# Kernel tuning notes

Measured on AMD Instinct MI355X. Metric: run time of the kernel, lower is better.

Reference implementation:

```python
import jax, jax.numpy as jnp
import numpy as np

B, S, D = 4, 4096, 256


def setup_inputs() -> dict:
    key = jax.random.key(0)
    k1, k2, k3 = jax.random.split(key, 3)
    x = jax.random.normal(k1, (B, S, D), dtype=jnp.float32)
    w_int = jax.random.randint(k2, (D, D), 0, 127, dtype=jnp.int32)  # quantized weight (out, in)
    scale = jax.random.uniform(k3, (D,), dtype=jnp.float32)          # per-output-channel scale
    return {"x": x, "w_int": w_int, "scale": scale}


def reference(x, w_int, scale):
    # self-attention: q = k = v = x, single head over feature dim D
    inv_sqrt_d = 1.0 / jnp.sqrt(jnp.asarray(D, dtype=x.dtype))
    scores = jnp.einsum('bqd,bkd->bqk', x, x) * inv_sqrt_d   # [B,S,S]
    probs = jax.nn.softmax(scores, axis=-1)
    attn = jnp.einsum('bqk,bkd->bqd', probs, x)              # [B,S,D]
    # quantized linear: dequantize then matmul (y = attn @ W^T)
    W = w_int.astype(x.dtype) * scale[:, None]               # [D_out, D_in]
    return jnp.einsum('bsd,od->bso', attn, W)
```

## Files before the change

### kernel.cpp

```cpp
#include <hip/hip_runtime.h>

typedef __bf16 bf16x8 __attribute__((ext_vector_type(8)));
typedef float f32x16 __attribute__((ext_vector_type(16)));
typedef unsigned short u16x8 __attribute__((ext_vector_type(8)));

constexpr int B = 4, S = 4096, D = 256;
constexpr float CSC = 0.09016844005556021f;

static __device__ __forceinline__ unsigned short f2bf(float f) {
  unsigned int u = __builtin_bit_cast(unsigned int, f);
  u = (u + 0x7fffu + ((u >> 16) & 1u)) >> 16;
  return (unsigned short)u;
}

static __device__ __forceinline__ float bf2f(unsigned short u) {
  unsigned int v = ((unsigned int)u) << 16;
  return __builtin_bit_cast(float, v);
}

static __device__ __forceinline__ unsigned int pk2bf(float lo, float hi) {
  unsigned int r;
  asm("v_cvt_pk_bf16_f32 %0, %1, %2" : "=v"(r) : "v"(lo), "v"(hi));
  return r;
}

static __device__ __forceinline__ void gld16(const void* g, void* l) {
  __builtin_amdgcn_global_load_lds(
      (const __attribute__((address_space(1))) unsigned int*)g,
      (__attribute__((address_space(3))) unsigned int*)l, 16, 0, 0);
}

#define FENCE_ALL()                                               \
  do {                                                            \
    asm volatile("s_waitcnt vmcnt(0) lgkmcnt(0)" ::: "memory");   \
    __builtin_amdgcn_s_barrier();                                 \
    asm volatile("" ::: "memory");                                \
  } while (0)

__global__ __launch_bounds__(256) void k_prep(const float* __restrict__ x,
                                              unsigned short* __restrict__ xbf,
                                              unsigned short* __restrict__ xK,
                                              unsigned short* __restrict__ xV) {
  __shared__ unsigned short T[64][72];
  __shared__ unsigned short R[64][72];
  int bid = blockIdx.x;
  int b = bid >> 8, rem = bid & 255;
  int s0 = (rem >> 2) * 64, d0 = (rem & 3) * 64;
  int j = threadIdx.x & 63, i0 = threadIdx.x >> 6;
#pragma unroll
  for (int k = 0; k < 16; ++k) {
    int i = k * 4 + i0;
    int idx = (b * S + s0 + i) * D + d0 + j;
    unsigned short v = f2bf(x[idx]);
    xbf[idx] = v;
    T[j][i] = v;
    R[i][j] = v;
  }
  __syncthreads();
  int t = s0 >> 6;
#pragma unroll
  for (int p = 0; p < 2; ++p) {
    int cc = p * 256 + threadIdx.x;
    int sl8 = cc >> 6, row = cc & 63;
    u16x8 v = *(const u16x8*)&R[row][sl8 * 8];
    int dg = d0 + sl8 * 8;
    int s = dg >> 4, hi = (dg >> 3) & 1;
    size_t off = ((((size_t)(b * 64 + t) * 16 + s) * 2 + hi) * 64 + row) * 8;
    *(u16x8*)(xK + off) = v;
  }
#pragma unroll
  for (int p = 0; p < 2; ++p) {
    int cc = p * 256 + threadIdx.x;
    int c = cc >> 7, hi = (cc >> 6) & 1, dl = cc & 63;
    u16x8 v = *(const u16x8*)&T[dl][c * 16 + hi * 8];
    size_t off = ((((size_t)(b * 64 + t) * 4 + c) * 2 + hi) * 256 + (d0 + dl)) * 8;
    *(u16x8*)(xV + off) = v;
  }
}

__global__ __launch_bounds__(256) void k_deqw(const int* __restrict__ w,
                                              unsigned short* __restrict__ wK) {
  int o = blockIdx.x, d = threadIdx.x;
  unsigned short v = f2bf((float)w[o * 256 + d]);
  wK[(((d >> 4) * 2 + ((d >> 3) & 1)) * 256 + o) * 8 + (d & 7)] = v;
}

__global__ __launch_bounds__(512, 2) void k_attn(const unsigned short* __restrict__ xbf,
                                                 const unsigned short* __restrict__ xK,
                                                 const unsigned short* __restrict__ xV,
                                                 unsigned short* __restrict__ PO0,
                                                 unsigned short* __restrict__ PO1,
                                                 float* __restrict__ ML) {
  __shared__ __align__(16) char smem[132096];

  int tid = threadIdx.x;
  int w = tid >> 6, lane = tid & 63;
  int q5 = lane & 31, hi = lane >> 5;
  int pair = w >> 1, dh = w & 1;

  int bid = blockIdx.x;
  int swz = (bid & 7) * 32 + (bid >> 3);
  int h = swz & 1;
  int qg = swz >> 1;
  int q0 = qg * 128;
  int bat = q0 >> 12;
  int qloc = q0 & (S - 1);

  const unsigned short* Xb = xbf + (size_t)bat * (S * D);
  int qw = qloc + pair * 32;

  bf16x8 qf[16];
#pragma unroll
  for (int s = 0; s < 16; ++s)
    qf[s] = *(const bf16x8*)(Xb + (qw + q5) * D + s * 16 + hi * 8);

  f32x16 acc[8];
#pragma unroll
  for (int dt = 0; dt < 8; ++dt)
#pragma unroll
    for (int j = 0; j < 16; ++j) acc[dt][j] = 0.f;
  float l_lane = 0.f;

  const char* xKb = (const char*)xK + (size_t)(bat * 64 + h * 32) * 32768;
  const char* xVb = (const char*)xV + (size_t)(bat * 64 + h * 32) * 32768;

  auto STAGE = [&](int itile, int bb) {
    char* Kd = smem + bb * 32768;
    char* Vd = smem + 65536 + bb * 32768;
    const char* srcK = xKb + (size_t)itile * 32768;
    const char* srcV = xVb + (size_t)itile * 32768;
#pragma unroll
    for (int i = 0; i < 4; ++i) {
      int off = (w * 2 + (i >> 1)) * 2048 + (i & 1) * 1024;
      gld16(srcK + off + lane * 16, Kd + off);
    }
#pragma unroll
    for (int i = 0; i < 4; ++i) {
      int off = (w >> 1) * 8192 + ((w & 1) * 4 + i) * 1024;
      gld16(srcV + off + lane * 16, Vd + off);
    }
  };

  STAGE(0, 0);
  FENCE_ALL();

  for (int it = 0; it < 32; ++it) {
    int bb = it & 1;
    if (it + 1 < 32) STAGE(it + 1, bb ^ 1);

    const char* Kt = smem + bb * 32768 + hi * 1024 + dh * 512 + q5 * 16;
    f32x16 st;
#pragma unroll
    for (int j = 0; j < 16; ++j) st[j] = 0.f;
    __builtin_amdgcn_s_setprio(1);
#pragma unroll
    for (int s = 0; s < 16; ++s) {
      bf16x8 kf = *(const bf16x8*)(Kt + s * 2048);
      st = __builtin_amdgcn_mfma_f32_32x32x16_bf16(kf, qf[s], st, 0, 0, 0);
    }
    __builtin_amdgcn_s_setprio(0);

    unsigned int pk[8];
    float ps = 0.f;
#pragma unroll
    for (int a = 0; a < 8; ++a) {
      float lo = exp2f(st[2 * a] * CSC);
      float hh = exp2f(st[2 * a + 1] * CSC);
      ps += lo + hh;
      pk[a] = pk2bf(lo, hh);
    }
    l_lane += ps;

    unsigned int a0 = pk[0], b0 = pk[2];
    unsigned int a1 = pk[1], b1 = pk[3];
    unsigned int a2 = pk[4], b2 = pk[6];
    unsigned int a3 = pk[5], b3 = pk[7];
    asm volatile("v_permlane32_swap_b32 %0, %1" : "+v"(a0), "+v"(b0));
    asm volatile("v_permlane32_swap_b32 %0, %1" : "+v"(a1), "+v"(b1));
    asm volatile("v_permlane32_swap_b32 %0, %1" : "+v"(a2), "+v"(b2));
    asm volatile("v_permlane32_swap_b32 %0, %1" : "+v"(a3), "+v"(b3));
    union PA { unsigned int u[4]; bf16x8 v; };
    PA pa0, pa1;
    pa0.u[0] = a0; pa0.u[1] = a1; pa0.u[2] = b0; pa0.u[3] = b1;
    pa1.u[0] = a2; pa1.u[1] = a3; pa1.u[2] = b2; pa1.u[3] = b3;

    __builtin_amdgcn_s_setprio(1);
#pragma unroll
    for (int s2i = 0; s2i < 2; ++s2i) {
      const char* Vt = smem + 65536 + bb * 32768 + (dh * 2 + s2i) * 8192 +
                       hi * 4096 + q5 * 16;
      bf16x8 pa = (s2i == 0) ? pa0.v : pa1.v;
#pragma unroll
      for (int dt = 0; dt < 8; ++dt) {
        bf16x8 vf = *(const bf16x8*)(Vt + dt * 512);
        acc[dt] = __builtin_amdgcn_mfma_f32_32x32x16_bf16(vf, pa, acc[dt], 0, 0, 0);
      }
    }
    __builtin_amdgcn_s_setprio(0);

    FENCE_ALL();
  }

  float lw = l_lane + __shfl_xor(l_lane, 32, 64);
  float* LX = (float*)(smem + 131072);
  if (lane < 32) LX[w * 32 + q5] = lw;
  __syncthreads();
  float l_tot = lw + LX[(w ^ 1) * 32 + q5];
  if (dh == 0 && lane < 32) {
    int row = q0 + pair * 32 + q5;
    ML[((size_t)h * 16384 + row) * 2 + 0] = 0.f;
    ML[((size_t)h * 16384 + row) * 2 + 1] = l_tot;
  }
  __syncthreads();

  unsigned short* Pb2 = (h == 0) ? PO0 : PO1;
#pragma unroll
  for (int rh = 0; rh < 2; ++rh) {
    float* slot = (float*)(smem + w * 16384);
#pragma unroll
    for (int dt4 = 0; dt4 < 4; ++dt4) {
#pragma unroll
      for (int r = 0; r < 16; ++r) {
        int dloc = dt4 * 32 + (r & 3) + 8 * (r >> 2) + 4 * hi;
        slot[dloc * 32 + q5] = acc[rh * 4 + dt4][r];
      }
    }
    __syncthreads();
    if (dh == rh) {
      const float* pslot = (const float*)(smem + (w ^ 1) * 16384);
#pragma unroll
      for (int dt4 = 0; dt4 < 4; ++dt4) {
#pragma unroll
        for (int r = 0; r < 16; ++r) {
          int dloc = dt4 * 32 + (r & 3) + 8 * (r >> 2) + 4 * hi;
          acc[rh * 4 + dt4][r] += pslot[dloc * 32 + q5];
        }
      }
      char* E = smem + w * 16384;
#pragma unroll
      for (int dt4 = 0; dt4 < 4; ++dt4) {
#pragma unroll
        for (int a = 0; a < 4; ++a) {
          int dl = dt4 * 32 + 8 * a + 4 * hi;
          *(unsigned int*)(E + q5 * 272 + dl * 2) =
              pk2bf(acc[rh * 4 + dt4][4 * a + 0], acc[rh * 4 + dt4][4 * a + 1]);
          *(unsigned int*)(E + q5 * 272 + dl * 2 + 4) =
              pk2bf(acc[rh * 4 + dt4][4 * a + 2], acc[rh * 4 + dt4][4 * a + 3]);
        }
      }
      asm volatile("s_waitcnt lgkmcnt(0)" ::: "memory");
#pragma unroll
      for (int i = 0; i < 8; ++i) {
        int qr = i * 4 + (lane >> 4);
        int ch = lane & 15;
        u16x8 v = *(const u16x8*)(E + qr * 272 + ch * 16);
        *(u16x8*)(Pb2 + (size_t)(q0 + pair * 32 + qr) * 256 + rh * 128 + ch * 8) = v;
      }
    }
    __syncthreads();
  }
}

__global__ __launch_bounds__(512, 2) void k_gemm(const unsigned short* __restrict__ PO0,
                                                 const unsigned short* __restrict__ PO1,
                                                 const float* __restrict__ ML,
                                                 const unsigned short* __restrict__ wK,
                                                 const float* __restrict__ scale,
                                                 float* __restrict__ out) {
  __shared__ __align__(16) char Wl[131072];
  int tid = threadIdx.x;
  int w = tid >> 6, lane = tid & 63;
  int q5 = lane & 31, hi = lane >> 5;
  int msub = w & 1, oq = w >> 1;
  int m0 = blockIdx.x * 64;

#pragma unroll
  for (int i = 0; i < 16; ++i) {
    int off = (i * 512 + tid) * 16;
    gld16((const char*)wK + off, Wl + off);
  }

  int row = m0 + msub * 32 + q5;
  float il = 1.f / (ML[(size_t)row * 2 + 1] + ML[((size_t)16384 + row) * 2 + 1]);

  bf16x8 af[16];
#pragma unroll
  for (int s = 0; s < 16; ++s) {
    u16x8 a0 = *(const u16x8*)(PO0 + (size_t)row * 256 + s * 16 + hi * 8);
    u16x8 a1 = *(const u16x8*)(PO1 + (size_t)row * 256 + s * 16 + hi * 8);
    union { unsigned int u[4]; bf16x8 v; } cv;
#pragma unroll
    for (int e = 0; e < 4; ++e) {
      float lo = (bf2f(a0[2 * e]) + bf2f(a1[2 * e])) * il;
      float hh = (bf2f(a0[2 * e + 1]) + bf2f(a1[2 * e + 1])) * il;
      cv.u[e] = pk2bf(lo, hh);
    }
    af[s] = cv.v;
  }

  asm volatile("s_waitcnt vmcnt(0)" ::: "memory");
  __builtin_amdgcn_s_barrier();

  f32x16 acc[2];
#pragma unroll
  for (int t = 0; t < 2; ++t)
#pragma unroll
    for (int j = 0; j < 16; ++j) acc[t][j] = 0.f;

#pragma unroll
  for (int t = 0; t < 2; ++t) {
    int obase = (oq * 2 + t) * 32;
    const char* Wt = Wl + hi * 4096 + (obase + q5) * 16;
#pragma unroll
    for (int s = 0; s < 16; ++s) {
      bf16x8 wf = *(const bf16x8*)(Wt + s * 8192);
      acc[t] = __builtin_amdgcn_mfma_f32_32x32x16_bf16(af[s], wf, acc[t], 0, 0, 0);
    }
  }

#pragma unroll
  for (int t = 0; t < 2; ++t) {
    int o = (oq * 2 + t) * 32 + q5;
    float sc = scale[o];
#pragma unroll
    for (int r = 0; r < 16; ++r) {
      int mr = m0 + msub * 32 + (r & 3) + 8 * (r >> 2) + 4 * hi;
      out[(size_t)mr * 256 + o] = acc[t][r] * sc;
    }
  }
}

extern "C" void kernel_launch(void* const* d_in, const int* in_sizes, int n_in,
                              void* d_out, int out_size, void* d_ws, size_t ws_size,
                              hipStream_t stream) {
  (void)in_sizes; (void)n_in; (void)out_size; (void)ws_size;
  const float* x = (const float*)d_in[0];
  const int* w_int = (const int*)d_in[1];
  const float* scale = (const float*)d_in[2];
  float* out = (float*)d_out;

  char* ws = (char*)d_ws;
  unsigned short* xbf = (unsigned short*)(ws);
  unsigned short* xK  = (unsigned short*)(ws + 8388608);
  unsigned short* xV  = (unsigned short*)(ws + 16777216);
  unsigned short* wK  = (unsigned short*)(ws + 25165824);
  float*          ML  = (float*)(ws + 25296896);
  unsigned short* PO0 = (unsigned short*)(ws + 25821184);
  unsigned short* PO1 = (unsigned short*)(ws + 34209792);

  k_prep<<<dim3(1024), dim3(256), 0, stream>>>(x, xbf, xK, xV);
  k_deqw<<<dim3(256), dim3(256), 0, stream>>>(w_int, wK);
  k_attn<<<dim3(256), dim3(512), 0, stream>>>(xbf, xK, xV, PO0, PO1, ML);
  k_gemm<<<dim3(256), dim3(512), 0, stream>>>(PO0, PO1, ML, wK, scale, out);
}
```

Before: 104.3 us.

## Software-pipeline QK and PV across tiles and drop separate bf16 x copy

Restructures the attention loop so K and V tiles are staged separately with partial vmcnt waits. The QK^T of tile t now overlaps with the PV of tile t-1, with softmax probabilities carried in registers between iterations. This is meant to hide load latency and keep the MFMA pipe busy instead of fully draining memory every iteration. It also removes the row-major bf16 copy of x and reads Q fragments from the K-layout buffer, saving one 8 MB write and its workspace. It adds register pressure from the carried probabilities and makes the fence and vmcnt accounting more delicate.

```diff
diff --git a/kernel.cpp b/kernel.cpp
--- a/kernel.cpp
+++ b/kernel.cpp
@@ -30,7 +30,25 @@
       (__attribute__((address_space(3))) unsigned int*)l, 16, 0, 0);
 }
 
-#define FENCE_ALL()                                               \
+#define FENCE_V4()                                                \
+  do {                                                            \
+    asm volatile("s_waitcnt vmcnt(4) lgkmcnt(0)" ::: "memory");   \
+    __builtin_amdgcn_s_barrier();                                 \
+    asm volatile("" ::: "memory");                                \
+  } while (0)
+#define FENCE_V8()                                                \
+  do {                                                            \
+    asm volatile("s_waitcnt vmcnt(8) lgkmcnt(0)" ::: "memory");   \
+    __builtin_amdgcn_s_barrier();                                 \
+    asm volatile("" ::: "memory");                                \
+  } while (0)
+#define FENCE_LG()                                                \
+  do {                                                            \
+    asm volatile("s_waitcnt lgkmcnt(0)" ::: "memory");            \
+    __builtin_amdgcn_s_barrier();                                 \
+    asm volatile("" ::: "memory");                                \
+  } while (0)
+#define FENCE_ALL0()                                              \
   do {                                                            \
     asm volatile("s_waitcnt vmcnt(0) lgkmcnt(0)" ::: "memory");   \
     __builtin_amdgcn_s_barrier();                                 \
@@ -38,7 +56,6 @@
   } while (0)
 
 __global__ __launch_bounds__(256) void k_prep(const float* __restrict__ x,
-                                              unsigned short* __restrict__ xbf,
                                               unsigned short* __restrict__ xK,
                                               unsigned short* __restrict__ xV) {
   __shared__ unsigned short T[64][72];
@@ -52,7 +69,6 @@
     int i = k * 4 + i0;
     int idx = (b * S + s0 + i) * D + d0 + j;
     unsigned short v = f2bf(x[idx]);
-    xbf[idx] = v;
     T[j][i] = v;
     R[i][j] = v;
   }
@@ -85,8 +101,7 @@
   wK[(((d >> 4) * 2 + ((d >> 3) & 1)) * 256 + o) * 8 + (d & 7)] = v;
 }
 
-__global__ __launch_bounds__(512, 2) void k_attn(const unsigned short* __restrict__ xbf,
-                                                 const unsigned short* __restrict__ xK,
+__global__ __launch_bounds__(512, 2) void k_attn(const unsigned short* __restrict__ xK,
                                                  const unsigned short* __restrict__ xV,
                                                  unsigned short* __restrict__ PO0,
                                                  unsigned short* __restrict__ PO1,
@@ -106,13 +121,12 @@
   int bat = q0 >> 12;
   int qloc = q0 & (S - 1);
 
-  const unsigned short* Xb = xbf + (size_t)bat * (S * D);
-  int qw = qloc + pair * 32;
-
+  int qrow = qloc + pair * 32 + q5;
+  const unsigned short* Qb =
+      xK + (size_t)(bat * 64 + (qrow >> 6)) * 16384 + hi * 512 + (qrow & 63) * 8;
   bf16x8 qf[16];
 #pragma unroll
-  for (int s = 0; s < 16; ++s)
-    qf[s] = *(const bf16x8*)(Xb + (qw + q5) * D + s * 16 + hi * 8);
+  for (int s = 0; s < 16; ++s) qf[s] = *(const bf16x8*)(Qb + s * 1024);
 
   f32x16 acc[8];
 #pragma unroll
@@ -120,20 +134,23 @@
 #pragma unroll
     for (int j = 0; j < 16; ++j) acc[dt][j] = 0.f;
   float l_lane = 0.f;
+  unsigned int paw[8];
 
   const char* xKb = (const char*)xK + (size_t)(bat * 64 + h * 32) * 32768;
   const char* xVb = (const char*)xV + (size_t)(bat * 64 + h * 32) * 32768;
 
-  auto STAGE = [&](int itile, int bb) {
+  auto STAGE_K = [&](int itile, int bb) {
     char* Kd = smem + bb * 32768;
-    char* Vd = smem + 65536 + bb * 32768;
     const char* srcK = xKb + (size_t)itile * 32768;
-    const char* srcV = xVb + (size_t)itile * 32768;
 #pragma unroll
     for (int i = 0; i < 4; ++i) {
       int off = (w * 2 + (i >> 1)) * 2048 + (i & 1) * 1024;
       gld16(srcK + off + lane * 16, Kd + off);
     }
+  };
+  auto STAGE_V = [&](int itile, int bb) {
+    char* Vd = smem + 65536 + bb * 32768;
+    const char* srcV = xVb + (size_t)itile * 32768;
 #pragma unroll
     for (int i = 0; i < 4; ++i) {
       int off = (w >> 1) * 8192 + ((w & 1) * 4 + i) * 1024;
@@ -141,15 +158,8 @@
     }
   };
 
-  STAGE(0, 0);
-  FENCE_ALL();
-
-  for (int it = 0; it < 32; ++it) {
-    int bb = it & 1;
-    if (it + 1 < 32) STAGE(it + 1, bb ^ 1);
-
+  auto QK = [&](int bb, f32x16& st) {
     const char* Kt = smem + bb * 32768 + hi * 1024 + dh * 512 + q5 * 16;
-    f32x16 st;
 #pragma unroll
     for (int j = 0; j < 16; ++j) st[j] = 0.f;
     __builtin_amdgcn_s_setprio(1);
@@ -159,7 +169,27 @@
       st = __builtin_amdgcn_mfma_f32_32x32x16_bf16(kf, qf[s], st, 0, 0, 0);
     }
     __builtin_amdgcn_s_setprio(0);
-
+  };
+  auto PV = [&](int bb) {
+    union PA { unsigned int u[4]; bf16x8 v; };
+    PA pa0, pa1;
+    pa0.u[0] = paw[0]; pa0.u[1] = paw[1]; pa0.u[2] = paw[2]; pa0.u[3] = paw[3];
+    pa1.u[0] = paw[4]; pa1.u[1] = paw[5]; pa1.u[2] = paw[6]; pa1.u[3] = paw[7];
+    __builtin_amdgcn_s_setprio(1);
+#pragma unroll
+    for (int s2i = 0; s2i < 2; ++s2i) {
+      const char* Vt = smem + 65536 + bb * 32768 + (dh * 2 + s2i) * 8192 +
+                       hi * 4096 + q5 * 16;
+      bf16x8 pa = (s2i == 0) ? pa0.v : pa1.v;
+#pragma unroll
+      for (int dt = 0; dt < 8; ++dt) {
+        bf16x8 vf = *(const bf16x8*)(Vt + dt * 512);
+        acc[dt] = __builtin_amdgcn_mfma_f32_32x32x16_bf16(vf, pa, acc[dt], 0, 0, 0);
+      }
+    }
+    __builtin_amdgcn_s_setprio(0);
+  };
+  auto SM = [&](const f32x16& st) {
     unsigned int pk[8];
     float ps = 0.f;
 #pragma unroll
@@ -170,7 +200,6 @@
       pk[a] = pk2bf(lo, hh);
     }
     l_lane += ps;
-
     unsigned int a0 = pk[0], b0 = pk[2];
     unsigned int a1 = pk[1], b1 = pk[3];
     unsigned int a2 = pk[4], b2 = pk[6];
@@ -179,27 +208,35 @@
     asm volatile("v_permlane32_swap_b32 %0, %1" : "+v"(a1), "+v"(b1));
     asm volatile("v_permlane32_swap_b32 %0, %1" : "+v"(a2), "+v"(b2));
     asm volatile("v_permlane32_swap_b32 %0, %1" : "+v"(a3), "+v"(b3));
-    union PA { unsigned int u[4]; bf16x8 v; };
-    PA pa0, pa1;
-    pa0.u[0] = a0; pa0.u[1] = a1; pa0.u[2] = b0; pa0.u[3] = b1;
-    pa1.u[0] = a2; pa1.u[1] = a3; pa1.u[2] = b2; pa1.u[3] = b3;
-
-    __builtin_amdgcn_s_setprio(1);
-#pragma unroll
-    for (int s2i = 0; s2i < 2; ++s2i) {
-      const char* Vt = smem + 65536 + bb * 32768 + (dh * 2 + s2i) * 8192 +
-                       hi * 4096 + q5 * 16;
-      bf16x8 pa = (s2i == 0) ? pa0.v : pa1.v;
-#pragma unroll
-      for (int dt = 0; dt < 8; ++dt) {
-        bf16x8 vf = *(const bf16x8*)(Vt + dt * 512);
-        acc[dt] = __builtin_amdgcn_mfma_f32_32x32x16_bf16(vf, pa, acc[dt], 0, 0, 0);
-      }
-    }
-    __builtin_amdgcn_s_setprio(0);
-
-    FENCE_ALL();
-  }
+    paw[0] = a0; paw[1] = a1; paw[2] = b0; paw[3] = b1;
+    paw[4] = a2; paw[5] = a3; paw[6] = b2; paw[7] = b3;
+  };
+
+  STAGE_K(0, 0);
+  STAGE_V(0, 0);
+  STAGE_K(1, 1);
+  FENCE_V8();
+  {
+    f32x16 st;
+    QK(0, st);
+    SM(st);
+  }
+  STAGE_V(1, 1);
+
+  for (int t = 1; t < 32; ++t) {
+    int cur = t & 1;
+    FENCE_V4();
+    if (t < 31) STAGE_K(t + 1, cur ^ 1);
+    f32x16 st;
+    QK(cur, st);
+    PV(cur ^ 1);
+    SM(st);
+    FENCE_LG();
+    if (t < 31) STAGE_V(t + 1, cur ^ 1);
+  }
+
+  FENCE_ALL0();
+  PV(1);
 
   float lw = l_lane + __shfl_xor(l_lane, 32, 64);
   float* LX = (float*)(smem + 131072);
@@ -340,16 +377,15 @@
   float* out = (float*)d_out;
 
   char* ws = (char*)d_ws;
-  unsigned short* xbf = (unsigned short*)(ws);
-  unsigned short* xK  = (unsigned short*)(ws + 8388608);
-  unsigned short* xV  = (unsigned short*)(ws + 16777216);
-  unsigned short* wK  = (unsigned short*)(ws + 25165824);
-  float*          ML  = (float*)(ws + 25296896);
-  unsigned short* PO0 = (unsigned short*)(ws + 25821184);
-  unsigned short* PO1 = (unsigned short*)(ws + 34209792);
-
-  k_prep<<<dim3(1024), dim3(256), 0, stream>>>(x, xbf, xK, xV);
+  unsigned short* xK  = (unsigned short*)(ws);
+  unsigned short* xV  = (unsigned short*)(ws + 8388608);
+  unsigned short* wK  = (unsigned short*)(ws + 16777216);
+  float*          ML  = (float*)(ws + 16908288);
+  unsigned short* PO0 = (unsigned short*)(ws + 17170432);
+  unsigned short* PO1 = (unsigned short*)(ws + 25559040);
+
+  k_prep<<<dim3(1024), dim3(256), 0, stream>>>(x, xK, xV);
   k_deqw<<<dim3(256), dim3(256), 0, stream>>>(w_int, wK);
-  k_attn<<<dim3(256), dim3(512), 0, stream>>>(xbf, xK, xV, PO0, PO1, ML);
+  k_attn<<<dim3(256), dim3(512), 0, stream>>>(xK, xV, PO0, PO1, ML);
   k_gemm<<<dim3(256), dim3(512), 0, stream>>>(PO0, PO1, ML, wK, scale, out);
 }
```

After: 101.3 us. 2.9% less time.
